# Optimization experiments

Measured on AMD Instinct MI355X. Metric: run time of the kernel, lower is better.

The kernel has to match this reference:

```python
import jax, jax.numpy as jnp
import numpy as np

LEAK = 0.2   # LeakyReLU slope in CVAE
T = 0.07     # MoCo temperature
TOPK = 2
DISK = 15


def _mlp2(x, Wa, ba, Wb, bb):
    # Linear -> ReLU -> Linear -> ReLU (MoCo encoders)
    return jax.nn.relu(jax.nn.relu(x @ Wa + ba) @ Wb + bb)


def setup_inputs() -> dict:
    key = jax.random.key(0)
    ks = jax.random.split(key, 32)
    B, R, V, F, L = 16384, 512, 1000, 300, 512

    def gn(k, shape, scale=0.05):
        return jax.random.normal(k, shape, dtype=jnp.float32) * scale

    inp = {}
    inp["logits"] = jax.random.normal(ks[0], (B, R), dtype=jnp.float32)
    inp["rels"] = jax.random.randint(ks[1], (R, 2), 0, V, dtype=jnp.int64)
    inp["rel_dict"] = jax.random.normal(ks[2], (V, F), dtype=jnp.float32)
    inp["eps1"] = jax.random.normal(ks[3], (B, L), dtype=jnp.float32)  # eps in ae.forward
    inp["eps2"] = jax.random.normal(ks[4], (B, L), dtype=jnp.float32)  # eps for z_
    # CVAE params (feature_size=300, class_size=300, latent_size=512)
    inp["W1"] = gn(ks[5], (F + F, 512)); inp["b1"] = jnp.zeros((512,), jnp.float32)
    inp["Wmu"] = gn(ks[6], (512, L));   inp["bmu"] = jnp.zeros((L,), jnp.float32)
    inp["Wls"] = gn(ks[7], (512, L));   inp["bls"] = jnp.zeros((L,), jnp.float32)
    inp["W3"] = gn(ks[8], (L + F, 512)); inp["b3"] = jnp.zeros((512,), jnp.float32)
    inp["W4"] = gn(ks[9], (512, F));    inp["b4"] = jnp.zeros((F,), jnp.float32)
    # MoCo encoder_inp (== encoder_k, since momentum update of identical params is a no-op)
    inp["iW1"] = gn(ks[10], (F, 512)); inp["ib1"] = jnp.zeros((512,), jnp.float32)
    inp["iW2"] = gn(ks[11], (512, 512)); inp["ib2"] = jnp.zeros((512,), jnp.float32)
    # MoCo encoder_z
    inp["zW1"] = gn(ks[12], (512, 512)); inp["zb1"] = jnp.zeros((512,), jnp.float32)
    inp["zW2"] = gn(ks[13], (512, 512)); inp["zb2"] = jnp.zeros((512,), jnp.float32)
    return inp


def reference(logits, rels, rel_dict, eps1, eps2,
              W1, b1, Wmu, bmu, Wls, bls, W3, b3, W4, b4,
              iW1, ib1, iW2, ib2, zW1, zb1, zW2, zb2):
    B = logits.shape[0]
    # sort descending / ascending over relation classes
    idx_desc = jnp.argsort(-logits, axis=1)
    idx_asc = jnp.argsort(logits, axis=1)
    top = idx_desc[:, :TOPK]        # [B,2]
    dis = idx_asc[:, :DISK]         # [B,15]

    keys = rels[:, 1]               # [R] indices into rel_dict
    # gathered features are all .detach()-ed in the original code
    pos1 = jax.lax.stop_gradient(rel_dict[keys[top[:, 0]]])   # [B,300]
    pos2 = jax.lax.stop_gradient(rel_dict[keys[top[:, 1]]])   # [B,300]
    neg = jax.lax.stop_gradient(rel_dict[keys[dis]])          # [B,15,300]

    # ---- CVAE forward (batched over B instead of the python loop) ----
    h1 = jax.nn.leaky_relu(jnp.concatenate([pos1, pos2], axis=1) @ W1 + b1, LEAK)
    mu = h1 @ Wmu + bmu              # [B,512]
    log_std = h1 @ Wls + bls         # [B,512]
    std = jnp.exp(log_std)
    z = mu + eps1 * std              # reparametrize inside ae.forward
    h3 = jax.nn.leaky_relu(jnp.concatenate([z, pos2], axis=1) @ W3 + b3, LEAK)
    recon = jnp.tanh(h3 @ W4 + b4)   # [B,300]

    recon_loss = jnp.sum((recon - pos1) ** 2)
    kl_loss = jnp.sum(-0.5 * (1.0 + 2.0 * log_std - mu ** 2 - jnp.exp(2.0 * log_std)))
    loss_vae = (recon_loss + kl_loss).reshape(1)

    z_ = mu + eps2 * std             # second, independent reparametrize for MoCo

    # ---- MoCo forward (batched) ----
    z_p = _mlp2(z_, zW1, zb1, zW2, zb2)                       # [B,512]
    pos_vec = _mlp2(pos1, iW1, ib1, iW2, ib2)                 # [B,512]
    # encoder_k params equal encoder_inp params (copied at init, momentum no-op); no grad
    neg_p = jax.lax.stop_gradient(_mlp2(neg, iW1, ib1, iW2, ib2))  # [B,15,512]

    pos = jnp.sum(z_p * pos_vec, axis=-1, keepdims=True)      # [B,1]
    negl = jnp.einsum('bd,bnd->bn', z_p, neg_p)               # [B,15]
    lg = jnp.concatenate([pos, negl], axis=1) / T             # [B,16]
    # cross entropy with label 0, mean over batch-of-1 then summed over the loop
    loss_csl = jnp.sum(-jax.nn.log_softmax(lg, axis=-1)[:, 0]).reshape(1)

    z_rel = jnp.concatenate([jnp.zeros((1, 512), z_p.dtype), z_p], axis=0)  # [B+1,512]
    return (loss_vae, loss_csl, z_rel)
```

## Files before the change

### kernel.cpp

```cpp
#include <hip/hip_runtime.h>
#include <math.h>

#define B_ 16384
#define R_ 512
#define V_ 1000
#define F_ 300
#define FP_ 320
#define L_ 512
#define H_ 512
#define LEAK_ 0.2f
#define TEMP_ 0.07f
#define DISK_ 15

#define NCSL_BLK (B_ / 4)
#define NKL_BLK  1024
#define NREC_BLK (3 * 128)

#define NT_ 11
#define FRONT_TOPK_BLK 3277
#define FRONT_GATHER_BLK R_
#define FRONT_TRANS_BLK (16 * 16 * NT_)

typedef short short8 __attribute__((ext_vector_type(8)));
typedef float float4v __attribute__((ext_vector_type(4)));

__device__ __forceinline__ float waveReduceSum(float v) {
#pragma unroll
    for (int off = 32; off; off >>= 1) v += __shfl_xor(v, off);
    return v;
}

__device__ __forceinline__ short f2bf(float f) {
    unsigned u = __float_as_uint(f);
    unsigned r = (u + 0x7FFFu + ((u >> 16) & 1u)) >> 16;
    return (short)r;
}

__device__ __forceinline__ void gld16(const short* g, short* l) {
    __builtin_amdgcn_global_load_lds(
        (const __attribute__((address_space(1))) void*)g,
        (__attribute__((address_space(3))) void*)l, 16, 0, 0);
}

__device__ __forceinline__ void xcd_swizzle(int& bx, int& by) {
    int gx = gridDim.x;
    int nwg = gx * gridDim.y;
    int wg = blockIdx.x + gx * blockIdx.y;
    int cpx = nwg >> 3;
    int swz = (wg & 7) * cpx + (wg >> 3);
    bx = swz % gx;
    by = swz / gx;
}

struct TransArgs {
    const float* W[NT_];
    short* Wt[NT_];
    int row_off[NT_];
    int K[NT_];
    int Kpad[NT_];
    int N[NT_];
    int Npad[NT_];
    int ilv[NT_];
};

__device__ void topk_body(int b, int lane, const float* __restrict__ logits,
                          int* __restrict__ top0, int* __restrict__ top1,
                          int* __restrict__ dis) {
    const float* lp = logits + (size_t)b * R_;
    float4 va = *(const float4*)&lp[lane * 8];
    float4 vb = *(const float4*)&lp[lane * 8 + 4];
    float v[8] = {va.x, va.y, va.z, va.w, vb.x, vb.y, vb.z, vb.w};
    unsigned u[8];
#pragma unroll
    for (int i = 0; i < 8; ++i) {
        int f = __float_as_int(v[i]);
        u[i] = (unsigned)f ^ ((unsigned)(f >> 31) | 0x80000000u);
    }
    unsigned long long t1 = 0ull, t2 = 0ull;
#pragma unroll
    for (int i = 0; i < 8; ++i) {
        unsigned long long k =
            ((unsigned long long)u[i] << 9) | (unsigned)(511 - (lane * 8 + i));
        if (k > t1) { t2 = t1; t1 = k; }
        else if (k > t2) t2 = k;
    }
#pragma unroll
    for (int off = 32; off; off >>= 1) {
        unsigned long long o1 = __shfl_xor(t1, off);
        unsigned long long o2 = __shfl_xor(t2, off);
        unsigned long long hi = t1 > o1 ? t1 : o1;
        unsigned long long lo = t1 > o1 ? o1 : t1;
        unsigned long long m2 = t2 > o2 ? t2 : o2;
        t1 = hi;
        t2 = lo > m2 ? lo : m2;
    }
    int i0 = 511 - (int)(t1 & 511u);
    int i1 = 511 - (int)(t2 & 511u);

    unsigned k32[8];
#pragma unroll
    for (int i = 0; i < 8; ++i) {
        int idx = lane * 8 + i;
        k32[i] = (u[i] & 0xFFFFFE00u) | (unsigned)idx;
        if (idx == i0 || idx == i1) k32[i] = 0xFFFFFFFFu;
    }
    unsigned lmin = k32[0];
#pragma unroll
    for (int i = 1; i < 8; ++i) lmin = min(lmin, k32[i]);
    int dloc[DISK_];
#pragma unroll
    for (int t = 0; t < DISK_; ++t) {
        unsigned w = lmin;
#pragma unroll
        for (int off = 32; off; off >>= 1) w = min(w, __shfl_xor(w, off));
        int idx = (int)(w & 0x1FFu);
        dloc[t] = idx;
        if ((idx >> 3) == lane) {
            k32[idx & 7] = 0xFFFFFFFFu;
            lmin = k32[0];
#pragma unroll
            for (int i = 1; i < 8; ++i) lmin = min(lmin, k32[i]);
        }
    }
    if (lane == 0) {
        top0[b] = i0; top1[b] = i1;
#pragma unroll
        for (int t = 0; t < DISK_; ++t) dis[b * DISK_ + t] = dloc[t];
    }
}

__global__ __launch_bounds__(320) void front_kernel(
    const float* __restrict__ logits, int* __restrict__ top0,
    int* __restrict__ top1, int* __restrict__ dis,
    const int* __restrict__ rels32, const float* __restrict__ rel_dict,
    float* __restrict__ d_table, short* __restrict__ dt, TransArgs ta) {
    __shared__ float tile[32][33];
    __shared__ int s_i64;
    int blk = blockIdx.x;
    int tid = threadIdx.x;

    if (blk < FRONT_TOPK_BLK) {
        int b = blk * 5 + (tid >> 6);
        if (b < B_) topk_body(b, tid & 63, logits, top0, top1, dis);
        return;
    }
    blk -= FRONT_TOPK_BLK;
    if (blk < FRONT_GATHER_BLK) {
        int r = blk;
        if (tid == 0) s_i64 = 1;
        __syncthreads();
        if (rels32[2 * tid + 1] != 0) s_i64 = 0;
        __syncthreads();
        int key = s_i64 ? rels32[4 * r + 2] : rels32[2 * r + 1];
        if (tid < F_) {
            float v = rel_dict[(size_t)key * F_ + tid];
            d_table[(size_t)r * F_ + tid] = v;
            dt[(size_t)r * FP_ + tid] = f2bf(v);
        } else {
            dt[(size_t)r * FP_ + tid] = 0;
        }
        return;
    }
    blk -= FRONT_GATHER_BLK;
    {
        int z = blk >> 8;
        int kx = blk & 15, ny = (blk >> 4) & 15;
        const float* W = ta.W[z];
        short* Wt = ta.Wt[z];
        int row_off = ta.row_off[z];
        int K = ta.K[z], Kpad = ta.Kpad[z], N = ta.N[z], Npad = ta.Npad[z];
        int ilv = ta.ilv[z];
        int k0 = kx * 32, n0 = ny * 32;
        bool live = (k0 < Kpad) && (n0 < Npad);
        bool act = live && (tid < 256);
        int tx = tid & 31, ty = tid >> 5;
        if (act) {
#pragma unroll
            for (int i = 0; i < 4; ++i) {
                int k = k0 + i * 8 + ty, n = n0 + tx;
                tile[i * 8 + ty][tx] =
                    (k < K && n < N) ? W[(size_t)(row_off + k) * N + n] : 0.f;
            }
        }
        __syncthreads();
        if (act) {
#pragma unroll
            for (int i = 0; i < 4; ++i) {
                int n = n0 + i * 8 + ty, k = k0 + tx;
                if (n < Npad && k < Kpad) {
                    int orow = (ilv >= 0) ? (ilv + 128 * (n >> 6) + (n & 63)) : n;
                    Wt[(size_t)orow * Kpad + k] = f2bf(tile[tx][i * 8 + ty]);
                }
            }
        }
    }
}

__global__ __launch_bounds__(256) void h1_kernel(
    const float* __restrict__ Pcat, const float* __restrict__ b1,
    const int* __restrict__ top0, const int* __restrict__ top1,
    short* __restrict__ h1b) {
    int blk = (blockIdx.x & 7) * 4096 + (blockIdx.x >> 3);
    int idx = blk * 256 + threadIdx.x;
    int b = idx >> 9, j = idx & 511;
    float v = Pcat[(size_t)top0[b] * 2048 + j] + Pcat[(size_t)top1[b] * 2048 + 512 + j] + b1[j];
    h1b[idx] = f2bf(v > 0.f ? v : LEAK_ * v);
}

__device__ __forceinline__ const short8* frag_at(const short* buf, int row, int cb) {
    return (const short8*)&buf[row * 64 + ((cb ^ (row & 7)) * 8)];
}

__device__ __forceinline__ void gemm_core(
    const short* __restrict__ A, const short* __restrict__ Wt,
    int row0, int col0, int tid, short* As0, short* Bs0,
    short* As1, short* Bs1, float4v (&acc)[2][8]) {
    const int K = 512;
    int lane = tid & 63, wv = tid >> 6;
    int lm = lane & 15, q = lane >> 4;
    int rsub = lane >> 3;
    int kswz = ((lane & 7) ^ rsub) * 8;
    int ga = row0 + wv * 8 + rsub;
    int gb = col0 + wv * 8 + rsub;
#pragma unroll
    for (int i = 0; i < 2; ++i)
#pragma unroll
        for (int j = 0; j < 8; ++j) acc[i][j] = {0.f, 0.f, 0.f, 0.f};

    auto STAGE = [&](short* lA, short* lB, int k0) {
#pragma unroll
        for (int j = 0; j < 4; ++j) {
            gld16(&A[(size_t)(ga + 32 * j) * K + k0 + kswz],
                  lA + (wv * 8 + 32 * j) * 64);
            gld16(&Wt[(size_t)(gb + 32 * j) * K + k0 + kswz],
                  lB + (wv * 8 + 32 * j) * 64);
        }
    };

    STAGE(As0, Bs0, 0);
#pragma unroll
    for (int t = 0; t < 8; ++t) {
        short* cA = (t & 1) ? As1 : As0;
        short* cB = (t & 1) ? Bs1 : Bs0;
        short* nA = (t & 1) ? As0 : As1;
        short* nB = (t & 1) ? Bs0 : Bs1;
        if (t < 7) {
            STAGE(nA, nB, (t + 1) * 64);
            asm volatile("s_waitcnt vmcnt(8)" ::: "memory");
        } else {
            asm volatile("s_waitcnt vmcnt(0)" ::: "memory");
        }
        __builtin_amdgcn_s_barrier();
        __builtin_amdgcn_sched_barrier(0);
#pragma unroll
        for (int kk = 0; kk < 2; ++kk) {
            short8 af[2], bf[8];
#pragma unroll
            for (int mt = 0; mt < 2; ++mt)
                af[mt] = *frag_at(cA, wv * 32 + mt * 16 + lm, kk * 4 + q);
#pragma unroll
            for (int nt = 0; nt < 8; ++nt)
                bf[nt] = *frag_at(cB, nt * 16 + lm, kk * 4 + q);
#pragma unroll
            for (int mt = 0; mt < 2; ++mt)
#pragma unroll
                for (int nt = 0; nt < 8; ++nt)
                    acc[mt][nt] = __builtin_amdgcn_mfma_f32_16x16x32_bf16(
                        af[mt], bf[nt], acc[mt][nt], 0, 0, 0);
        }
        __builtin_amdgcn_s_barrier();
    }
}

template <int MODE>
__device__ __forceinline__ void epi_std(
    float4v (&acc)[2][8], int row0, int col0, int tid, void* C,
    const float* __restrict__ bias, const float* __restrict__ table,
    int tld, const int* __restrict__ rowsel) {
    int lane = tid & 63, wv = tid >> 6;
    int lm = lane & 15, q = lane >> 4;
#pragma unroll
    for (int mt = 0; mt < 2; ++mt)
#pragma unroll
        for (int r = 0; r < 4; ++r) {
            int grow = row0 + wv * 32 + mt * 16 + q * 4 + r;
            int trow = (MODE == 1) ? rowsel[grow] : 0;
#pragma unroll
            for (int nt = 0; nt < 8; ++nt) {
                int gcol = col0 + nt * 16 + lm;
                float v = acc[mt][nt][r] + bias[gcol];
                if (MODE == 1) {
                    v += table[(size_t)trow * tld + gcol];
                    v = v > 0.f ? v : LEAK_ * v;
                } else {
                    v = v > 0.f ? v : 0.f;
                }
                if (MODE == 4)
                    ((float*)C)[(size_t)grow * 512 + gcol] = v;
                else
                    ((short*)C)[(size_t)grow * 512 + gcol] = f2bf(v);
            }
        }
}

__device__ __forceinline__ void epi_recon(
    float4v (&acc)[2][8], int row0, int col0, int tid,
    const float* __restrict__ b4, const float* __restrict__ d_table,
    const int* __restrict__ top0, float* __restrict__ p_rec, int pidx,
    float* sred) {
    int lane = tid & 63, wv = tid >> 6;
    int lm = lane & 15, q = lane >> 4;
    float lsum = 0.f;
#pragma unroll
    for (int mt = 0; mt < 2; ++mt)
#pragma unroll
        for (int r = 0; r < 4; ++r) {
            int grow = row0 + wv * 32 + mt * 16 + q * 4 + r;
            int trow = top0[grow];
#pragma unroll
            for (int nt = 0; nt < 8; ++nt) {
                int gcol = col0 + nt * 16 + lm;
                if (gcol < F_) {
                    float v = tanhf(acc[mt][nt][r] + b4[gcol]);
                    float d = v - d_table[(size_t)trow * F_ + gcol];
                    lsum += d * d;
                }
            }
        }
    lsum = waveReduceSum(lsum);
    if (lane == 0) sred[wv] = lsum;
    __syncthreads();
    if (tid == 0) p_rec[pidx] = sred[0] + sred[1] + sred[2] + sred[3];
}

__global__ __launch_bounds__(256) void gemm_muls(
    const short* __restrict__ A, const short* __restrict__ Wt,
    short* __restrict__ Cz, short* __restrict__ Cz2,
    const float* __restrict__ bmu, const float* __restrict__ bls,
    const float* __restrict__ eps1, const float* __restrict__ eps2,
    float* __restrict__ p_kl) {
    __shared__ __align__(16) short As[2][128 * 64];
    __shared__ __align__(16) short Bs[2][128 * 64];
    __shared__ float sred[4];
    int tid = threadIdx.x;
    int bx, by;
    xcd_swizzle(bx, by);
    int row0 = by * 128, col0 = bx * 128;
    float4v acc[2][8];
    gemm_core(A, Wt, row0, col0, tid, As[0], Bs[0], As[1], Bs[1], acc);

    int lane = tid & 63, wv = tid >> 6;
    int lm = lane & 15, q = lane >> 4;
    float kl = 0.f;
#pragma unroll
    for (int mt = 0; mt < 2; ++mt) {
#pragma unroll
        for (int r = 0; r < 4; ++r) {
            int grow = row0 + wv * 32 + mt * 16 + q * 4 + r;
#pragma unroll
            for (int jj = 0; jj < 4; ++jj) {
                int j = (col0 >> 1) + jj * 16 + lm;
                float m = acc[mt][jj][r] + bmu[j];
                float lsv = acc[mt][jj + 4][r] + bls[j];
                float s = __expf(lsv);
                size_t ix = (size_t)grow * 512 + j;
                Cz[ix]  = f2bf(m + eps1[ix] * s);
                Cz2[ix] = f2bf(m + eps2[ix] * s);
                kl += -0.5f * (1.f + 2.f * lsv - m * m - s * s);
            }
        }
    }
    kl = waveReduceSum(kl);
    if (lane == 0) sred[wv] = kl;
    __syncthreads();
    if (tid == 0)
        p_kl[bx + gridDim.x * by] = sred[0] + sred[1] + sred[2] + sred[3];
}

__global__ __launch_bounds__(256) void dual12_kernel(
    const short* __restrict__ zA, const short* __restrict__ Wt3,
    short* __restrict__ h3out, const float* __restrict__ b3,
    const float* __restrict__ Ptab, const int* __restrict__ top1,
    const short* __restrict__ zpA, const short* __restrict__ Wtz1,
    short* __restrict__ tout, const float* __restrict__ zb1,
    const short* __restrict__ ipreA, const short* __restrict__ Wti2,
    float* __restrict__ ipostC, const float* __restrict__ ib2,
    int jobSel) {
    __shared__ __align__(16) short As[2][128 * 64];
    __shared__ __align__(16) short Bs[2][128 * 64];
    int tid = threadIdx.x;
    int k = blockIdx.x & 7, m = blockIdx.x >> 3;
    int job, bx, by;
    if (jobSel >= 0) {
        job = jobSel;
        if (job == 2) { int idx = k * 2 + m; bx = idx & 3; by = idx >> 2; }
        else { bx = m & 3; by = 16 * k + (m >> 2); }
    } else {
        if (m < 64)       { job = 0; bx = m & 3; by = 16 * k + (m >> 2); }
        else if (m < 128) { int mm = m - 64; job = 1; bx = mm & 3; by = 16 * k + (mm >> 2); }
        else              { int mm = m - 128; job = 2; int idx = k * 2 + mm; bx = idx & 3; by = idx >> 2; }
    }
    int row0 = by * 128, col0 = bx * 128;
    float4v acc[2][8];
    if (job == 0) {
        gemm_core(zA, Wt3, row0, col0, tid, As[0], Bs[0], As[1], Bs[1], acc);
        epi_std<1>(acc, row0, col0, tid, h3out, b3, Ptab, 2048, top1);
    } else if (job == 1) {
        gemm_core(zpA, Wtz1, row0, col0, tid, As[0], Bs[0], As[1], Bs[1], acc);
        epi_std<2>(acc, row0, col0, tid, tout, zb1, nullptr, 0, nullptr);
    } else {
        gemm_core(ipreA, Wti2, row0, col0, tid, As[0], Bs[0], As[1], Bs[1], acc);
        epi_std<4>(acc, row0, col0, tid, ipostC, ib2, nullptr, 0, nullptr);
    }
}

__global__ __launch_bounds__(256) void dual34_kernel(
    const short* __restrict__ tA, const short* __restrict__ Wtz2,
    float* __restrict__ zpout, const float* __restrict__ zb2,
    const short* __restrict__ h3A, const short* __restrict__ Wt4,
    const float* __restrict__ b4, const float* __restrict__ d_table,
    const int* __restrict__ top0, float* __restrict__ p_rec, int jobSel) {
    __shared__ __align__(16) short As[2][128 * 64];
    __shared__ __align__(16) short Bs[2][128 * 64];
    __shared__ float sred[4];
    int tid = threadIdx.x;
    int k = blockIdx.x & 7, m = blockIdx.x >> 3;
    int job, bx, by;
    if (jobSel >= 0) {
        job = jobSel;
        if (job == 0) { bx = m & 3; by = 16 * k + (m >> 2); }
        else          { bx = m % 3; by = 16 * k + m / 3; }
    } else {
        if (m < 64) { job = 0; bx = m & 3; by = 16 * k + (m >> 2); }
        else        { int mm = m - 64; job = 1; bx = mm % 3; by = 16 * k + mm / 3; }
    }
    float4v acc[2][8];
    if (job == 0) {
        int row0 = by * 128, col0 = bx * 128;
        gemm_core(tA, Wtz2, row0, col0, tid, As[0], Bs[0], As[1], Bs[1], acc);
        epi_std<4>(acc, row0, col0, tid, zpout, zb2, nullptr, 0, nullptr);
    } else {
        int row0 = by * 128, col0 = bx * 128;
        gemm_core(h3A, Wt4, row0, col0, tid, As[0], Bs[0], As[1], Bs[1], acc);
        epi_recon(acc, row0, col0, tid, b4, d_table, top0, p_rec,
                  bx + 3 * by, sred);
    }
}

template <int KK>
__global__ __launch_bounds__(256) void gemm_mfma64(
    const short* __restrict__ A, const short* __restrict__ Wt,
    float* __restrict__ C, int ldc, const float* __restrict__ ib1,
    short* __restrict__ ipre_out) {
    __shared__ __align__(16) short Asl[2][64][40];
    __shared__ __align__(16) short Bsl[2][64][40];
    int tid = threadIdx.x;
    int lane = tid & 63, wv = tid >> 6;
    int lm = lane & 15, q = lane >> 4;
    int bx, by;
    xcd_swizzle(bx, by);
    int row0 = by * 64;
    int col0 = bx * 64;

    float4v acc[4];
#pragma unroll
    for (int j = 0; j < 4; ++j) acc[j] = {0.f, 0.f, 0.f, 0.f};

    uint4 aReg, bReg;
    int ar = tid >> 2, ak = (tid & 3) * 8;

    auto loadG = [&](int k0) {
        aReg = *(const uint4*)&A[(size_t)(row0 + ar) * KK + k0 + ak];
        bReg = *(const uint4*)&Wt[(size_t)(col0 + ar) * KK + k0 + ak];
    };
    auto storeL = [&](int p) {
        *(uint4*)&Asl[p][ar][ak] = aReg;
        *(uint4*)&Bsl[p][ar][ak] = bReg;
    };

    int p = 0;
    loadG(0);
    storeL(0);
    for (int k0 = 0; k0 < KK; k0 += 32) {
        __syncthreads();
        bool more = (k0 + 32) < KK;
        if (more) loadG(k0 + 32);
        short8 af, bfr[4];
        af = *(const short8*)&Asl[p][wv * 16 + lm][q * 8];
#pragma unroll
        for (int nt = 0; nt < 4; ++nt)
            bfr[nt] = *(const short8*)&Bsl[p][nt * 16 + lm][q * 8];
#pragma unroll
        for (int nt = 0; nt < 4; ++nt)
            acc[nt] = __builtin_amdgcn_mfma_f32_16x16x32_bf16(
                af, bfr[nt], acc[nt], 0, 0, 0);
        if (more) { p ^= 1; storeL(p); }
    }

#pragma unroll
    for (int r = 0; r < 4; ++r) {
        int grow = row0 + wv * 16 + q * 4 + r;
#pragma unroll
        for (int nt = 0; nt < 4; ++nt) {
            int gcol = col0 + nt * 16 + lm;
            float v = acc[nt][r];
            C[(size_t)grow * ldc + gcol] = v;
            if (gcol >= 1536) {
                int j = gcol - 1536;
                float w = v + ib1[j];
                ipre_out[(size_t)grow * 512 + j] = f2bf(w > 0.f ? w : 0.f);
            }
        }
    }
}

__global__ __launch_bounds__(256) void csl_kernel(
    const float* __restrict__ zp, const float* __restrict__ ipost,
    const int* __restrict__ top0, const int* __restrict__ dis,
    float* __restrict__ partial_csl) {
    __shared__ float sred[4];
    int blk = (blockIdx.x & 7) * 512 + (blockIdx.x >> 3);
    int w = threadIdx.x >> 6, lane = threadIdx.x & 63;
    int b = blk * 4 + w;
    const float* zr = zp + (size_t)b * 512;
    float z[8];
#pragma unroll
    for (int i = 0; i < 8; ++i) z[i] = zr[i * 64 + lane];
    int cand[16];
    cand[0] = top0[b];
#pragma unroll
    for (int n = 0; n < DISK_; ++n) cand[n + 1] = dis[b * DISK_ + n];
    float s[16];
#pragma unroll
    for (int c = 0; c < 16; ++c) {
        const float* ip = ipost + (size_t)cand[c] * 512;
        float a = 0.f;
#pragma unroll
        for (int i = 0; i < 8; ++i) a += z[i] * ip[i * 64 + lane];
        s[c] = a;
    }
#pragma unroll
    for (int off = 32; off; off >>= 1) {
        float o[16];
#pragma unroll
        for (int c = 0; c < 16; ++c) o[c] = __shfl_xor(s[c], off);
#pragma unroll
        for (int c = 0; c < 16; ++c) s[c] += o[c];
    }
    if (lane == 0) {
        float m = s[0];
#pragma unroll
        for (int c = 1; c < 16; ++c) m = fmaxf(m, s[c]);
        float se = 0.f;
#pragma unroll
        for (int c = 0; c < 16; ++c) se += __expf((s[c] - m) / TEMP_);
        sred[w] = -((s[0] - m) / TEMP_ - __logf(se));
    }
    __syncthreads();
    if (threadIdx.x == 0)
        partial_csl[blk] = sred[0] + sred[1] + sred[2] + sred[3];
}

__global__ __launch_bounds__(256) void finalize_kernel(
    const float* __restrict__ pkl, const float* __restrict__ prec,
    const float* __restrict__ pcsl, float* __restrict__ out) {
    __shared__ float red[4][2];
    int tid = threadIdx.x;
    out[2 + tid] = 0.f;
    out[2 + 256 + tid] = 0.f;
    float a0 = 0.f, a1 = 0.f;
    for (int i = tid; i < NKL_BLK; i += 256) a0 += pkl[i];
    for (int i = tid; i < NREC_BLK; i += 256) a0 += prec[i];
    for (int i = tid; i < NCSL_BLK; i += 256) a1 += pcsl[i];
    a0 = waveReduceSum(a0);
    a1 = waveReduceSum(a1);
    int lane = tid & 63, w = tid >> 6;
    if (lane == 0) { red[w][0] = a0; red[w][1] = a1; }
    __syncthreads();
    if (tid == 0) out[0] = red[0][0] + red[1][0] + red[2][0] + red[3][0];
    if (tid == 1) out[1] = red[0][1] + red[1][1] + red[2][1] + red[3][1];
}

extern "C" void kernel_launch(void* const* d_in, const int* in_sizes, int n_in,
                              void* d_out, int out_size, void* d_ws, size_t ws_size,
                              hipStream_t stream) {
    const float* logits  = (const float*)d_in[0];
    const int*   rels    = (const int*)d_in[1];
    const float* rel_dict= (const float*)d_in[2];
    const float* eps1    = (const float*)d_in[3];
    const float* eps2    = (const float*)d_in[4];
    const float* W1  = (const float*)d_in[5];
    const float* b1  = (const float*)d_in[6];
    const float* Wmu = (const float*)d_in[7];
    const float* bmu = (const float*)d_in[8];
    const float* Wls = (const float*)d_in[9];
    const float* bls = (const float*)d_in[10];
    const float* W3  = (const float*)d_in[11];
    const float* b3  = (const float*)d_in[12];
    const float* W4  = (const float*)d_in[13];
    const float* b4  = (const float*)d_in[14];
    const float* iW1 = (const float*)d_in[15];
    const float* ib1 = (const float*)d_in[16];
    const float* iW2 = (const float*)d_in[17];
    const float* ib2 = (const float*)d_in[18];
    const float* zW1 = (const float*)d_in[19];
    const float* zb1 = (const float*)d_in[20];
    const float* zW2 = (const float*)d_in[21];
    const float* zb2 = (const float*)d_in[22];
    float* out = (float*)d_out;

    char* wsp = (char*)d_ws;
    size_t off = 0;
    auto alloc = [&](size_t bytes) { void* p = wsp + off; off += (bytes + 255) & ~(size_t)255; return p; };
    int*   top0    = (int*)alloc(B_ * 4);
    int*   top1    = (int*)alloc(B_ * 4);
    int*   dis     = (int*)alloc(B_ * DISK_ * 4);
    float* d_table = (float*)alloc((size_t)R_ * F_ * 4);
    short* dt      = (short*)alloc((size_t)R_ * FP_ * 2);
    short* Wcat_t  = (short*)alloc((size_t)2048 * FP_ * 2);
    float* Pcat    = (float*)alloc((size_t)R_ * 2048 * 4);
    short* ipre    = (short*)alloc((size_t)R_ * H_ * 2);
    float* ipost   = (float*)alloc((size_t)R_ * H_ * 4);
    short* Wt_muls = (short*)alloc((size_t)1024 * 512 * 2);
    short* Wt_3    = (short*)alloc((size_t)512 * 512 * 2);
    short* Wt_z1   = (short*)alloc((size_t)512 * 512 * 2);
    short* Wt_z2   = (short*)alloc((size_t)512 * 512 * 2);
    short* Wt_4    = (short*)alloc((size_t)384 * 512 * 2);
    short* Wt_i2   = (short*)alloc((size_t)512 * 512 * 2);
    short* bfA     = (short*)alloc((size_t)B_ * H_ * 2);
    short* bfB     = (short*)alloc((size_t)B_ * H_ * 2);
    short* bfC     = (short*)alloc((size_t)B_ * H_ * 2);
    float* p_csl   = (float*)alloc(NCSL_BLK * 4);
    float* p_kl    = (float*)alloc(NKL_BLK * 4);
    float* p_rec   = (float*)alloc(NREC_BLK * 4);
    size_t bfD_bytes = (size_t)B_ * H_ * 2;
    bool merged = (off + bfD_bytes + 256) <= ws_size;
    short* bfD = merged ? (short*)alloc(bfD_bytes) : bfB;

    TransArgs ta;
    auto set = [&](int i, const float* W, short* Wt, int ro, int K, int Kp, int N, int Np, int ilv) {
        ta.W[i] = W; ta.Wt[i] = Wt; ta.row_off[i] = ro; ta.K[i] = K;
        ta.Kpad[i] = Kp; ta.N[i] = N; ta.Npad[i] = Np; ta.ilv[i] = ilv;
    };
    set(0, Wmu, Wt_muls, 0, 512, 512, 512, 512, 0);
    set(1, Wls, Wt_muls, 0, 512, 512, 512, 512, 64);
    set(2, W3,  Wt_3,  0, 512, 512, 512, 512, -1);
    set(3, zW1, Wt_z1, 0, 512, 512, 512, 512, -1);
    set(4, zW2, Wt_z2, 0, 512, 512, 512, 512, -1);
    set(5, W4,  Wt_4,  0, 512, 512, 300, 384, -1);
    set(6, W1,  Wcat_t,              0,  F_, FP_, 512, 512, -1);
    set(7, W1,  Wcat_t + 512 * FP_,  F_, F_, FP_, 512, 512, -1);
    set(8, W3,  Wcat_t + 1024 * FP_, L_, F_, FP_, 512, 512, -1);
    set(9, iW1, Wcat_t + 1536 * FP_, 0,  F_, FP_, 512, 512, -1);
    set(10, iW2, Wt_i2, 0, 512, 512, 512, 512, -1);

    front_kernel<<<FRONT_TOPK_BLK + FRONT_GATHER_BLK + FRONT_TRANS_BLK,
                   320, 0, stream>>>(
        logits, top0, top1, dis, rels, rel_dict, d_table, dt, ta);

    gemm_mfma64<FP_><<<dim3(32, 8), 256, 0, stream>>>(
        dt, Wcat_t, Pcat, 2048, ib1, ipre);
    h1_kernel<<<B_ * H_ / 256, 256, 0, stream>>>(Pcat, b1, top0, top1, bfA);

    gemm_muls<<<dim3(8, 128), 256, 0, stream>>>(
        bfA, Wt_muls, bfB, bfC, bmu, bls, eps1, eps2, p_kl);

    if (merged) {
        dual12_kernel<<<1040, 256, 0, stream>>>(
            bfB, Wt_3, bfA, b3, Pcat + 1024, top1,
            bfC, Wt_z1, bfD, zb1,
            ipre, Wt_i2, ipost, ib2, -1);
        dual34_kernel<<<896, 256, 0, stream>>>(
            bfD, Wt_z2, out + 2 + L_, zb2,
            bfA, Wt_4, b4, d_table, top0, p_rec, -1);
    } else {
        dual12_kernel<<<512, 256, 0, stream>>>(
            bfB, Wt_3, bfA, b3, Pcat + 1024, top1,
            bfC, Wt_z1, bfD, zb1, ipre, Wt_i2, ipost, ib2, 0);
        dual12_kernel<<<512, 256, 0, stream>>>(
            bfB, Wt_3, bfA, b3, Pcat + 1024, top1,
            bfC, Wt_z1, bfD, zb1, ipre, Wt_i2, ipost, ib2, 1);
        dual12_kernel<<<16, 256, 0, stream>>>(
            bfB, Wt_3, bfA, b3, Pcat + 1024, top1,
            bfC, Wt_z1, bfD, zb1, ipre, Wt_i2, ipost, ib2, 2);
        dual34_kernel<<<512, 256, 0, stream>>>(
            bfD, Wt_z2, out + 2 + L_, zb2,
            bfA, Wt_4, b4, d_table, top0, p_rec, 0);
        dual34_kernel<<<384, 256, 0, stream>>>(
            bfD, Wt_z2, out + 2 + L_, zb2,
            bfA, Wt_4, b4, d_table, top0, p_rec, 1);
    }

    csl_kernel<<<NCSL_BLK, 256, 0, stream>>>(out + 2 + L_, ipost, top0, dis, p_csl);
    finalize_kernel<<<1, 256, 0, stream>>>(p_kl, p_rec, p_csl, out);
}
```

Baseline: 367.0 us.

## Move top-k selection into Pcat GEMM launch and vectorize h1 gather

Top-k/bottom-k selection over logits now runs in extra blocks of the Pcat GEMM launch instead of the front kernel. The small 256-block GEMM therefore overlaps with the memory-bound top-k work, and the front kernel becomes shorter. The h1 kernel is also vectorized so each thread handles 8 elements with float4 loads and a short8 store. Top-k blocks are now 4 rows per 256-thread block instead of 5 per 320, which changes occupancy characteristics.

```diff
diff --git a/kernel.cpp b/kernel.cpp
--- a/kernel.cpp
+++ b/kernel.cpp
@@ -17,9 +17,10 @@
 #define NREC_BLK (3 * 128)
 
 #define NT_ 11
-#define FRONT_TOPK_BLK 3277
 #define FRONT_GATHER_BLK R_
 #define FRONT_TRANS_BLK (16 * 16 * NT_)
+#define PCAT_BLK 256
+#define TOPK_BLK (B_ / 4)
 
 typedef short short8 __attribute__((ext_vector_type(8)));
 typedef float float4v __attribute__((ext_vector_type(4)));
@@ -130,8 +131,6 @@
 }
 
 __global__ __launch_bounds__(320) void front_kernel(
-    const float* __restrict__ logits, int* __restrict__ top0,
-    int* __restrict__ top1, int* __restrict__ dis,
     const int* __restrict__ rels32, const float* __restrict__ rel_dict,
     float* __restrict__ d_table, short* __restrict__ dt, TransArgs ta) {
     __shared__ float tile[32][33];
@@ -139,12 +138,6 @@
     int blk = blockIdx.x;
     int tid = threadIdx.x;
 
-    if (blk < FRONT_TOPK_BLK) {
-        int b = blk * 5 + (tid >> 6);
-        if (b < B_) topk_body(b, tid & 63, logits, top0, top1, dis);
-        return;
-    }
-    blk -= FRONT_TOPK_BLK;
     if (blk < FRONT_GATHER_BLK) {
         int r = blk;
         if (tid == 0) s_i64 = 1;
@@ -196,15 +189,109 @@
     }
 }
 
+template <int KK>
+__global__ __launch_bounds__(256) void pcat_topk_kernel(
+    const short* __restrict__ A, const short* __restrict__ Wt,
+    float* __restrict__ C, int ldc, const float* __restrict__ ib1,
+    short* __restrict__ ipre_out,
+    const float* __restrict__ logits, int* __restrict__ top0,
+    int* __restrict__ top1, int* __restrict__ dis) {
+    __shared__ __align__(16) short Asl[2][64][40];
+    __shared__ __align__(16) short Bsl[2][64][40];
+    int tid = threadIdx.x;
+
+    if (blockIdx.x >= PCAT_BLK) {
+        int b = (blockIdx.x - PCAT_BLK) * 4 + (tid >> 6);
+        topk_body(b, tid & 63, logits, top0, top1, dis);
+        return;
+    }
+
+    int wg = blockIdx.x;
+    int swz = (wg & 7) * 32 + (wg >> 3);
+    int bx = swz & 31, by = swz >> 5;
+    int lane = tid & 63, wv = tid >> 6;
+    int lm = lane & 15, q = lane >> 4;
+    int row0 = by * 64;
+    int col0 = bx * 64;
+
+    float4v acc[4];
+#pragma unroll
+    for (int j = 0; j < 4; ++j) acc[j] = {0.f, 0.f, 0.f, 0.f};
+
+    uint4 aReg, bReg;
+    int ar = tid >> 2, ak = (tid & 3) * 8;
+
+    auto loadG = [&](int k0) {
+        aReg = *(const uint4*)&A[(size_t)(row0 + ar) * KK + k0 + ak];
+        bReg = *(const uint4*)&Wt[(size_t)(col0 + ar) * KK + k0 + ak];
+    };
+    auto storeL = [&](int p) {
+        *(uint4*)&Asl[p][ar][ak] = aReg;
+        *(uint4*)&Bsl[p][ar][ak] = bReg;
+    };
+
+    int p = 0;
+    loadG(0);
+    storeL(0);
+    for (int k0 = 0; k0 < KK; k0 += 32) {
+        __syncthreads();
+        bool more = (k0 + 32) < KK;
+        if (more) loadG(k0 + 32);
+        short8 af, bfr[4];
+        af = *(const short8*)&Asl[p][wv * 16 + lm][q * 8];
+#pragma unroll
+        for (int nt = 0; nt < 4; ++nt)
+            bfr[nt] = *(const short8*)&Bsl[p][nt * 16 + lm][q * 8];
+#pragma unroll
+        for (int nt = 0; nt < 4; ++nt)
+            acc[nt] = __builtin_amdgcn_mfma_f32_16x16x32_bf16(
+                af, bfr[nt], acc[nt], 0, 0, 0);
+        if (more) { p ^= 1; storeL(p); }
+    }
+
+#pragma unroll
+    for (int r = 0; r < 4; ++r) {
+        int grow = row0 + wv * 16 + q * 4 + r;
+#pragma unroll
+        for (int nt = 0; nt < 4; ++nt) {
+            int gcol = col0 + nt * 16 + lm;
+            float v = acc[nt][r];
+            C[(size_t)grow * ldc + gcol] = v;
+            if (gcol >= 1536) {
+                int j = gcol - 1536;
+                float w = v + ib1[j];
+                ipre_out[(size_t)grow * 512 + j] = f2bf(w > 0.f ? w : 0.f);
+            }
+        }
+    }
+}
+
 __global__ __launch_bounds__(256) void h1_kernel(
     const float* __restrict__ Pcat, const float* __restrict__ b1,
     const int* __restrict__ top0, const int* __restrict__ top1,
     short* __restrict__ h1b) {
-    int blk = (blockIdx.x & 7) * 4096 + (blockIdx.x >> 3);
-    int idx = blk * 256 + threadIdx.x;
+    int blk = (blockIdx.x & 7) * 512 + (blockIdx.x >> 3);
+    int idx = blk * 2048 + threadIdx.x * 8;
     int b = idx >> 9, j = idx & 511;
-    float v = Pcat[(size_t)top0[b] * 2048 + j] + Pcat[(size_t)top1[b] * 2048 + 512 + j] + b1[j];
-    h1b[idx] = f2bf(v > 0.f ? v : LEAK_ * v);
+    const float* p0 = &Pcat[(size_t)top0[b] * 2048 + j];
+    const float* p1 = &Pcat[(size_t)top1[b] * 2048 + 512 + j];
+    float4 a0 = *(const float4*)p0;
+    float4 a1 = *(const float4*)(p0 + 4);
+    float4 c0 = *(const float4*)p1;
+    float4 c1 = *(const float4*)(p1 + 4);
+    float4 d0 = *(const float4*)&b1[j];
+    float4 d1 = *(const float4*)&b1[j + 4];
+    float t[8] = {a0.x + c0.x + d0.x, a0.y + c0.y + d0.y,
+                  a0.z + c0.z + d0.z, a0.w + c0.w + d0.w,
+                  a1.x + c1.x + d1.x, a1.y + c1.y + d1.y,
+                  a1.z + c1.z + d1.z, a1.w + c1.w + d1.w};
+    short8 o;
+#pragma unroll
+    for (int i = 0; i < 8; ++i) {
+        float v = t[i];
+        o[i] = f2bf(v > 0.f ? v : LEAK_ * v);
+    }
+    *(short8*)&h1b[idx] = o;
 }
 
 __device__ __forceinline__ const short8* frag_at(const short* buf, int row, int cb) {
@@ -444,73 +531,6 @@
         gemm_core(h3A, Wt4, row0, col0, tid, As[0], Bs[0], As[1], Bs[1], acc);
         epi_recon(acc, row0, col0, tid, b4, d_table, top0, p_rec,
                   bx + 3 * by, sred);
-    }
-}
-
-template <int KK>
-__global__ __launch_bounds__(256) void gemm_mfma64(
-    const short* __restrict__ A, const short* __restrict__ Wt,
-    float* __restrict__ C, int ldc, const float* __restrict__ ib1,
-    short* __restrict__ ipre_out) {
-    __shared__ __align__(16) short Asl[2][64][40];
-    __shared__ __align__(16) short Bsl[2][64][40];
-    int tid = threadIdx.x;
-    int lane = tid & 63, wv = tid >> 6;
-    int lm = lane & 15, q = lane >> 4;
-    int bx, by;
-    xcd_swizzle(bx, by);
-    int row0 = by * 64;
-    int col0 = bx * 64;
-
-    float4v acc[4];
-#pragma unroll
-    for (int j = 0; j < 4; ++j) acc[j] = {0.f, 0.f, 0.f, 0.f};
-
-    uint4 aReg, bReg;
-    int ar = tid >> 2, ak = (tid & 3) * 8;
-
-    auto loadG = [&](int k0) {
-        aReg = *(const uint4*)&A[(size_t)(row0 + ar) * KK + k0 + ak];
-        bReg = *(const uint4*)&Wt[(size_t)(col0 + ar) * KK + k0 + ak];
-    };
-    auto storeL = [&](int p) {
-        *(uint4*)&Asl[p][ar][ak] = aReg;
-        *(uint4*)&Bsl[p][ar][ak] = bReg;
-    };
-
-    int p = 0;
-    loadG(0);
-    storeL(0);
-    for (int k0 = 0; k0 < KK; k0 += 32) {
-        __syncthreads();
-        bool more = (k0 + 32) < KK;
-        if (more) loadG(k0 + 32);
-        short8 af, bfr[4];
-        af = *(const short8*)&Asl[p][wv * 16 + lm][q * 8];
-#pragma unroll
-        for (int nt = 0; nt < 4; ++nt)
-            bfr[nt] = *(const short8*)&Bsl[p][nt * 16 + lm][q * 8];
-#pragma unroll
-        for (int nt = 0; nt < 4; ++nt)
-            acc[nt] = __builtin_amdgcn_mfma_f32_16x16x32_bf16(
-                af, bfr[nt], acc[nt], 0, 0, 0);
-        if (more) { p ^= 1; storeL(p); }
-    }
-
-#pragma unroll
-    for (int r = 0; r < 4; ++r) {
-        int grow = row0 + wv * 16 + q * 4 + r;
-#pragma unroll
-        for (int nt = 0; nt < 4; ++nt) {
-            int gcol = col0 + nt * 16 + lm;
-            float v = acc[nt][r];
-            C[(size_t)grow * ldc + gcol] = v;
-            if (gcol >= 1536) {
-                int j = gcol - 1536;
-                float w = v + ib1[j];
-                ipre_out[(size_t)grow * 512 + j] = f2bf(w > 0.f ? w : 0.f);
-            }
-        }
     }
 }
 
@@ -654,13 +674,13 @@
     set(9, iW1, Wcat_t + 1536 * FP_, 0,  F_, FP_, 512, 512, -1);
     set(10, iW2, Wt_i2, 0, 512, 512, 512, 512, -1);
 
-    front_kernel<<<FRONT_TOPK_BLK + FRONT_GATHER_BLK + FRONT_TRANS_BLK,
-                   320, 0, stream>>>(
-        logits, top0, top1, dis, rels, rel_dict, d_table, dt, ta);
-
-    gemm_mfma64<FP_><<<dim3(32, 8), 256, 0, stream>>>(
-        dt, Wcat_t, Pcat, 2048, ib1, ipre);
-    h1_kernel<<<B_ * H_ / 256, 256, 0, stream>>>(Pcat, b1, top0, top1, bfA);
+    front_kernel<<<FRONT_GATHER_BLK + FRONT_TRANS_BLK, 320, 0, stream>>>(
+        rels, rel_dict, d_table, dt, ta);
+
+    pcat_topk_kernel<FP_><<<PCAT_BLK + TOPK_BLK, 256, 0, stream>>>(
+        dt, Wcat_t, Pcat, 2048, ib1, ipre, logits, top0, top1, dis);
+
+    h1_kernel<<<4096, 256, 0, stream>>>(Pcat, b1, top0, top1, bfA);
 
     gemm_muls<<<dim3(8, 128), 256, 0, stream>>>(
         bfA, Wt_muls, bfB, bfC, bmu, bls, eps1, eps2, p_kl);
```

Measured after the change: 348.3 us. 1.05x faster.
